# Kernel optimization log

Hardware: AMD Instinct MI355X
Metric: run time of the kernel (lower is better)

The kernel has to match this reference:

```python
import jax, jax.numpy as jnp
import numpy as np

B, N, F_IN, F_OUT, H = 4, 2048, 256, 256, 4
NEG_INF = -1e9
EDGE_PROB = 0.05
LEAKY_SLOPE = 0.2  # tf.nn.leaky_relu default alpha


def setup_inputs() -> dict:
    key = jax.random.key(0)
    k_x, k_m, k_w, k_a, k_b = jax.random.split(key, 5)
    inputs = jax.random.normal(k_x, (B, N, F_IN), dtype=jnp.float32)
    # bias: additive adjacency mask, 0 on edges / -1e9 off-edges (standard GAT)
    u = jax.random.uniform(k_m, (B, N, N), dtype=jnp.float32)
    bias = jnp.where(u < EDGE_PROB, 0.0, NEG_INF).astype(jnp.float32)
    # self-loops so every softmax row has at least one valid entry
    bias = bias.at[:, jnp.arange(N), jnp.arange(N)].set(0.0)
    # per-head learned params (uniform [0,1) init as in the original)
    W = jax.random.uniform(k_w, (H, F_IN, F_OUT), dtype=jnp.float32)
    a = jax.random.uniform(k_a, (H, F_OUT), dtype=jnp.float32)
    b = jax.random.uniform(k_b, (H, F_OUT), dtype=jnp.float32)
    return {"inputs": inputs, "bias": bias, "W": W, "a": a, "b": b}


def reference(inputs, bias, W, a, b):
    # transformed: [H, B, N, F_OUT]
    t = jnp.einsum('bnf,hfo->hbno', inputs, W) + b[:, None, None, :]
    # per-node score s = t @ a : [H, B, N]
    s = jnp.einsum('hbno,ho->hbn', t, a)
    # weights[i,j] = s[i] + s[j]  (weights + transpose)
    w = s[..., :, None] + s[..., None, :]  # [H, B, N, N]
    coefs = jax.nn.softmax(jax.nn.leaky_relu(w, negative_slope=LEAKY_SLOPE) + bias, axis=-1)
    heads = jnp.einsum('hbnm,hbmo->hbno', coefs, t)  # [H, B, N, F_OUT]
    return jnp.mean(heads, axis=0)  # (1/num_heads) * add_n(heads)
```

## Files before the change

### kernel.cpp

```cpp
#include <hip/hip_runtime.h>
#include <hip/hip_bf16.h>

#define H 4
#define BB 4
#define NN 2048
#define FIN 256
#define FOUT 256
#define M_TOT (BB*NN)
#define LEAKY 0.2f

typedef float f32x4 __attribute__((ext_vector_type(4)));
typedef short s16x8 __attribute__((ext_vector_type(8)));

static __device__ __forceinline__ short f2bf(float f) {
    return __builtin_bit_cast(short, __float2bfloat16(f));
}
static __device__ __forceinline__ float bf2f(short u) {
    unsigned x = ((unsigned)(unsigned short)u) << 16;
    return __builtin_bit_cast(float, x);
}

__global__ __launch_bounds__(256) void k_wt(const float* __restrict__ W, short* __restrict__ WT) {
    __shared__ float lds[64][65];
    int bid = blockIdx.x;
    int h = bid >> 4, kt = (bid >> 2) & 3, ot = bid & 3;
    int kb = kt * 64, ob = ot * 64;
    int tx = threadIdx.x & 63, ty = threadIdx.x >> 6;
#pragma unroll
    for (int r = 0; r < 16; ++r) {
        int k_l = ty + r * 4;
        lds[tx][k_l] = W[(size_t)(h * FIN + kb + k_l) * FOUT + ob + tx];
    }
    __syncthreads();
#pragma unroll
    for (int r = 0; r < 16; ++r) {
        int o_l = ty + r * 4;
        WT[(size_t)(h * FOUT + ob + o_l) * FIN + kb + tx] = f2bf(lds[o_l][tx]);
    }
}

__global__ __launch_bounds__(256) void k_q(const float* __restrict__ W, const float* __restrict__ a,
                                           float* __restrict__ q) {
    int wv = (blockIdx.x * 256 + threadIdx.x) >> 6;
    int lane = threadIdx.x & 63;
    int h = wv >> 8, f = wv & 255;
    float4 w4 = *(const float4*)(W + (size_t)(h * FIN + f) * FOUT + lane * 4);
    float4 a4 = *(const float4*)(a + h * FOUT + lane * 4);
    float d = w4.x * a4.x + w4.y * a4.y + w4.z * a4.z + w4.w * a4.w;
#pragma unroll
    for (int off = 32; off; off >>= 1) d += __shfl_xor(d, off);
    if (lane == 0) q[h * FIN + f] = d;
}

__global__ __launch_bounds__(256) void k_c(const float* __restrict__ bvec, const float* __restrict__ a,
                                           float* __restrict__ c) {
    int h = threadIdx.x >> 6, lane = threadIdx.x & 63;
    float4 b4 = *(const float4*)(bvec + h * FOUT + lane * 4);
    float4 a4 = *(const float4*)(a + h * FOUT + lane * 4);
    float d = b4.x * a4.x + b4.y * a4.y + b4.z * a4.z + b4.w * a4.w;
#pragma unroll
    for (int off = 32; off; off >>= 1) d += __shfl_xor(d, off);
    if (lane == 0) c[h] = d;
}

__global__ __launch_bounds__(256) void k_s(const float* __restrict__ X, const float* __restrict__ q,
                                           const float* __restrict__ c, float* __restrict__ s,
                                           short* __restrict__ Xbf) {
    int m = blockIdx.x * 4 + (threadIdx.x >> 6);
    int lane = threadIdx.x & 63;
    float4 xv = *(const float4*)(X + (size_t)m * FIN + lane * 4);
    short4 xb;
    xb.x = f2bf(xv.x); xb.y = f2bf(xv.y); xb.z = f2bf(xv.z); xb.w = f2bf(xv.w);
    *(short4*)(Xbf + (size_t)m * FIN + lane * 4) = xb;
#pragma unroll
    for (int h = 0; h < H; ++h) {
        float4 qv = *(const float4*)(q + h * FIN + lane * 4);
        float d = xv.x * qv.x + xv.y * qv.y + xv.z * qv.z + xv.w * qv.w;
#pragma unroll
        for (int off = 32; off; off >>= 1) d += __shfl_xor(d, off);
        if (lane == 0) s[h * M_TOT + m] = d + c[h];
    }
}

__global__ __launch_bounds__(256) void k_mask(const float* __restrict__ bias, unsigned* __restrict__ mask) {
    size_t t = (size_t)blockIdx.x * 256 + threadIdx.x;
    const float* p = bias + t * 32;
    unsigned bits = 0;
#pragma unroll
    for (int k = 0; k < 8; ++k) {
        float4 v = *(const float4*)(p + k * 4);
        bits |= (v.x > -1.f ? 1u : 0u) << (k * 4 + 0);
        bits |= (v.y > -1.f ? 1u : 0u) << (k * 4 + 1);
        bits |= (v.z > -1.f ? 1u : 0u) << (k * 4 + 2);
        bits |= (v.w > -1.f ? 1u : 0u) << (k * 4 + 3);
    }
    mask[t] = bits;
}

__global__ __launch_bounds__(256) void k_gemm_t(const short* __restrict__ WT, const short* __restrict__ Xbf,
                                                const float* __restrict__ bvec, short* __restrict__ tT) {
    int h = blockIdx.z;
    int ob = blockIdx.y * 64;
    int mb = blockIdx.x * 128;
    int lane = threadIdx.x & 63, w = threadIdx.x >> 6;
    int r16 = lane & 15, g = lane >> 4;
    int mw = mb + w * 32;
    f32x4 acc[4][2] = {};
    for (int k = 0; k < FIN; k += 32) {
        s16x8 afr[4], bfr[2];
#pragma unroll
        for (int fa = 0; fa < 4; ++fa)
            afr[fa] = *(const s16x8*)(WT + (size_t)(h * FOUT + ob + fa * 16 + r16) * FIN + k + g * 8);
#pragma unroll
        for (int fb = 0; fb < 2; ++fb)
            bfr[fb] = *(const s16x8*)(Xbf + (size_t)(mw + fb * 16 + r16) * FIN + k + g * 8);
#pragma unroll
        for (int fa = 0; fa < 4; ++fa)
#pragma unroll
            for (int fb = 0; fb < 2; ++fb)
                acc[fa][fb] = __builtin_amdgcn_mfma_f32_16x16x32_bf16(afr[fa], bfr[fb], acc[fa][fb], 0, 0, 0);
    }
#pragma unroll
    for (int fa = 0; fa < 4; ++fa) {
#pragma unroll
        for (int r = 0; r < 4; ++r) {
            int o = ob + fa * 16 + g * 4 + r;
            float bv = bvec[h * FOUT + o];
#pragma unroll
            for (int fb = 0; fb < 2; ++fb) {
                int m = mw + fb * 16 + r16;
                tT[(size_t)(h * FOUT + o) * M_TOT + m] = f2bf(acc[fa][fb][r] + bv);
            }
        }
    }
}

__global__ __launch_bounds__(512, 4) void k_attn(const short* __restrict__ tT, const float* __restrict__ s,
                                                 const unsigned* __restrict__ mask, short* __restrict__ OT) {
    __shared__ short lds_t[256 * 64];
    __shared__ float lds_ml[4][64][2];

    int flat = blockIdx.x + 32 * (blockIdx.y + 4 * blockIdx.z);
    int swz = (flat & 7) * 64 + (flat >> 3);
    int qt = swz & 31, b = (swz >> 5) & 3, h = swz >> 7;
    int ib = qt * 64;

    int tid = threadIdx.x;
    int lane = tid & 63, w = tid >> 6;
    int r16 = lane & 15, g = lane >> 4;
    int q16 = w >> 1, par = w & 1;
    int i_loc = ib + q16 * 16 + r16;
    size_t gm = (size_t)b * NN;

    float s_i = s[h * M_TOT + gm + i_loc];
    const float* srow = s + h * M_TOT + gm;
    const unsigned* mrowp = mask + ((size_t)(gm + i_loc)) * (NN / 32);

    int o_st = tid >> 1, hf = tid & 1;
    const short* src = tT + ((size_t)(h * FOUT) + o_st) * M_TOT + gm + hf * 32;
    int rd_base = r16 * 64 + ((((par << 2) + g) ^ (r16 & 7)) << 3);

    f32x4 acc[16] = {};
    float mrow = -1e9f, lrow = 0.f;

    s16x8 rv0 = *(const s16x8*)(src);
    s16x8 rv1 = *(const s16x8*)(src + 8);
    s16x8 rv2 = *(const s16x8*)(src + 16);
    s16x8 rv3 = *(const s16x8*)(src + 24);

    for (int it = 0; it < 32; ++it) {
        int wb = o_st * 64;
        int sw = (o_st & 7);
        *(s16x8*)(lds_t + wb + ((((hf << 2) + 0) ^ sw) << 3)) = rv0;
        *(s16x8*)(lds_t + wb + ((((hf << 2) + 1) ^ sw) << 3)) = rv1;
        *(s16x8*)(lds_t + wb + ((((hf << 2) + 2) ^ sw) << 3)) = rv2;
        *(s16x8*)(lds_t + wb + ((((hf << 2) + 3) ^ sw) << 3)) = rv3;
        __syncthreads();

        if (it + 1 < 32) {
            const short* nsrc = src + (it + 1) * 64;
            rv0 = *(const s16x8*)(nsrc);
            rv1 = *(const s16x8*)(nsrc + 8);
            rv2 = *(const s16x8*)(nsrc + 16);
            rv3 = *(const s16x8*)(nsrc + 24);
        }

        int jw = it * 64 + par * 32;
        unsigned mw = mrowp[jw >> 5];
        float4 sj0 = *(const float4*)(srow + jw + g * 8);
        float4 sj1 = *(const float4*)(srow + jw + g * 8 + 4);
        float sjv[8] = {sj0.x, sj0.y, sj0.z, sj0.w, sj1.x, sj1.y, sj1.z, sj1.w};
        float sc[8];
#pragma unroll
        for (int e = 0; e < 8; ++e) {
            float wv = s_i + sjv[e];
            float lv = wv > 0.f ? wv : LEAKY * wv;
            sc[e] = ((mw >> (g * 8 + e)) & 1u) ? lv : -1e9f;
        }
        float tmax = sc[0];
#pragma unroll
        for (int e = 1; e < 8; ++e) tmax = fmaxf(tmax, sc[e]);
        tmax = fmaxf(tmax, __shfl_xor(tmax, 16));
        tmax = fmaxf(tmax, __shfl_xor(tmax, 32));

        if (!__all(tmax <= mrow + 8.f)) {
            float mnew = fmaxf(mrow, tmax);
            float scale = __expf(mrow - mnew);
            lrow *= scale;
#pragma unroll
            for (int f = 0; f < 16; ++f) {
                acc[f][0] *= scale; acc[f][1] *= scale;
                acc[f][2] *= scale; acc[f][3] *= scale;
            }
            mrow = mnew;
        }

        float ps = 0.f;
        s16x8 pb;
#pragma unroll
        for (int e = 0; e < 8; ++e) {
            float p = ((mw >> (g * 8 + e)) & 1u) ? __expf(sc[e] - mrow) : 0.f;
            ps += p;
            pb[e] = f2bf(p);
        }
        ps += __shfl_xor(ps, 16);
        ps += __shfl_xor(ps, 32);
        lrow += ps;

#pragma unroll
        for (int f = 0; f < 16; ++f) {
            s16x8 af = *(const s16x8*)(lds_t + f * 1024 + rd_base);
            acc[f] = __builtin_amdgcn_mfma_f32_16x16x32_bf16(af, pb, acc[f], 0, 0, 0);
        }
        __syncthreads();
    }

    if (par) {
        lds_ml[q16][lane][0] = mrow;
        lds_ml[q16][lane][1] = lrow;
    }
    __syncthreads();
    float f0 = 0.f, f1 = 0.f;
    if (!par) {
        float m1 = lds_ml[q16][lane][0];
        float l1 = lds_ml[q16][lane][1];
        float ms = fmaxf(mrow, m1);
        float s0 = __expf(mrow - ms);
        float s1 = __expf(m1 - ms);
        float ln = lrow * s0 + l1 * s1;
        float inv = 1.f / ln;
        f0 = s0 * inv; f1 = s1 * inv;
    }
    f32x4* accst = (f32x4*)lds_t;
#pragma unroll
    for (int r = 0; r < 2; ++r) {
        if (par) {
#pragma unroll
            for (int f = 0; f < 8; ++f) accst[(q16 * 8 + f) * 64 + lane] = acc[r * 8 + f];
        }
        __syncthreads();
        if (!par) {
#pragma unroll
            for (int f = 0; f < 8; ++f) {
                f32x4 v1 = accst[(q16 * 8 + f) * 64 + lane];
                f32x4 v = acc[r * 8 + f] * f0 + v1 * f1;
                int fg = r * 8 + f;
#pragma unroll
                for (int rr = 0; rr < 4; ++rr) {
                    int o = fg * 16 + g * 4 + rr;
                    OT[(size_t)(h * FOUT + o) * M_TOT + gm + i_loc] = f2bf(v[rr]);
                }
            }
        }
        __syncthreads();
    }
}

__global__ __launch_bounds__(256) void k_reduce(const short* __restrict__ OT, float* __restrict__ out) {
    __shared__ float lds[32][72];
    int mb = blockIdx.x * 64, obt = blockIdx.y * 32;
    int tid = threadIdx.x;
    {
        int o_l = tid >> 3;
        int m_l = (tid & 7) * 8;
        float acc[8] = {};
#pragma unroll
        for (int h = 0; h < H; ++h) {
            s16x8 v = *(const s16x8*)(OT + (size_t)(h * FOUT + obt + o_l) * M_TOT + mb + m_l);
#pragma unroll
            for (int e = 0; e < 8; ++e) acc[e] += bf2f(v[e]);
        }
#pragma unroll
        for (int e = 0; e < 8; ++e) lds[o_l][m_l + e] = acc[e] * 0.25f;
    }
    __syncthreads();
    {
        int m_l = tid >> 2;
        int o_l = (tid & 3) * 8;
        float4 v0, v1;
        v0.x = lds[o_l + 0][m_l]; v0.y = lds[o_l + 1][m_l];
        v0.z = lds[o_l + 2][m_l]; v0.w = lds[o_l + 3][m_l];
        v1.x = lds[o_l + 4][m_l]; v1.y = lds[o_l + 5][m_l];
        v1.z = lds[o_l + 6][m_l]; v1.w = lds[o_l + 7][m_l];
        float* dst = out + (size_t)(mb + m_l) * FOUT + obt + o_l;
        *(float4*)dst = v0;
        *(float4*)(dst + 4) = v1;
    }
}

extern "C" void kernel_launch(void* const* d_in, const int* in_sizes, int n_in,
                              void* d_out, int out_size, void* d_ws, size_t ws_size,
                              hipStream_t stream) {
    const float* X    = (const float*)d_in[0];
    const float* bias = (const float*)d_in[1];
    const float* W    = (const float*)d_in[2];
    const float* a    = (const float*)d_in[3];
    const float* bvec = (const float*)d_in[4];
    float* out = (float*)d_out;

    char* ws = (char*)d_ws;
    short*    Xbf  = (short*)ws;
    short*    WT   = (short*)(ws + (4u << 20));
    float*    q    = (float*)(ws + (4u << 20) + (768u << 10));
    float*    c    = q + H * FIN;
    float*    s    = (float*)(ws + (5u << 20));
    short*    tT   = (short*)(ws + (6u << 20));
    short*    OT   = (short*)(ws + (22u << 20));
    unsigned* mask = (unsigned*)(ws + (38u << 20));

    k_wt<<<64, 256, 0, stream>>>(W, WT);
    k_q<<<256, 256, 0, stream>>>(W, a, q);
    k_c<<<1, 256, 0, stream>>>(bvec, a, c);
    k_s<<<2048, 256, 0, stream>>>(X, q, c, s, Xbf);
    k_mask<<<2048, 256, 0, stream>>>(bias, mask);
    k_gemm_t<<<dim3(64, 4, 4), 256, 0, stream>>>(WT, Xbf, bvec, tT);
    k_attn<<<dim3(32, 4, 4), 512, 0, stream>>>(tT, s, mask, OT);
    k_reduce<<<dim3(128, 8), 256, 0, stream>>>(OT, out);
}
```

Baseline: 142.8 us.

## Double-buffer attention K tiles via direct global-to-LDS loads with pre-swizzled layout

The GEMM now writes the transformed features into a pre-tiled, XOR-swizzled slab layout so the attention kernel can copy each 64-column tile straight into LDS with global_load_lds. Those copies are double-buffered so the next tile loads while MFMAs run on the current one. The block shrinks from 512 to 256 threads, and each wave now handles two 16-row query groups that share each LDS fragment load. This raises register pressure (two accumulator sets), uses more LDS for the double buffer, and lowers occupancy.

After: 139.3 us. -2.5%, faster.

```diff
diff --git a/kernel.cpp b/kernel.cpp
--- a/kernel.cpp
+++ b/kernel.cpp
@@ -1,5 +1,6 @@
 #include <hip/hip_runtime.h>
 #include <hip/hip_bf16.h>
+#include <stdint.h>
 
 #define H 4
 #define BB 4
@@ -11,6 +12,7 @@
 
 typedef float f32x4 __attribute__((ext_vector_type(4)));
 typedef short s16x8 __attribute__((ext_vector_type(8)));
+typedef unsigned int u32;
 
 static __device__ __forceinline__ short f2bf(float f) {
     return __builtin_bit_cast(short, __float2bfloat16(f));
@@ -18,6 +20,16 @@
 static __device__ __forceinline__ float bf2f(short u) {
     unsigned x = ((unsigned)(unsigned short)u) << 16;
     return __builtin_bit_cast(float, x);
+}
+static __device__ __forceinline__ void glds16(const void* g, void* l) {
+    __builtin_amdgcn_global_load_lds(
+        (const __attribute__((address_space(1))) u32*)(g),
+        (__attribute__((address_space(3))) u32*)(l), 16, 0, 0);
+}
+
+static __device__ __forceinline__ size_t tts_addr(int h, int b, int o, int j) {
+    return ((size_t)((h * 4 + b) * 32 + (j >> 6))) * 16384
+         + o * 64 + ((((j >> 3) & 7) ^ (o & 7)) << 3) + (j & 7);
 }
 
 __global__ __launch_bounds__(256) void k_wt(const float* __restrict__ W, short* __restrict__ WT) {
@@ -98,7 +110,7 @@
 }
 
 __global__ __launch_bounds__(256) void k_gemm_t(const short* __restrict__ WT, const short* __restrict__ Xbf,
-                                                const float* __restrict__ bvec, short* __restrict__ tT) {
+                                                const float* __restrict__ bvec, short* __restrict__ tTs) {
     int h = blockIdx.z;
     int ob = blockIdx.y * 64;
     int mb = blockIdx.x * 128;
@@ -129,16 +141,17 @@
 #pragma unroll
             for (int fb = 0; fb < 2; ++fb) {
                 int m = mw + fb * 16 + r16;
-                tT[(size_t)(h * FOUT + o) * M_TOT + m] = f2bf(acc[fa][fb][r] + bv);
+                int bb = m >> 11, j = m & 2047;
+                tTs[tts_addr(h, bb, o, j)] = f2bf(acc[fa][fb][r] + bv);
             }
         }
     }
 }
 
-__global__ __launch_bounds__(512, 4) void k_attn(const short* __restrict__ tT, const float* __restrict__ s,
+__global__ __launch_bounds__(256, 2) void k_attn(const short* __restrict__ tTs, const float* __restrict__ s,
                                                  const unsigned* __restrict__ mask, short* __restrict__ OT) {
-    __shared__ short lds_t[256 * 64];
-    __shared__ float lds_ml[4][64][2];
+    __shared__ short buf[2][16384];
+    __shared__ float lds_ml[2][64][4];
 
     int flat = blockIdx.x + 32 * (blockIdx.y + 4 * blockIdx.z);
     int swz = (flat & 7) * 64 + (flat >> 3);
@@ -148,131 +161,139 @@
     int tid = threadIdx.x;
     int lane = tid & 63, w = tid >> 6;
     int r16 = lane & 15, g = lane >> 4;
-    int q16 = w >> 1, par = w & 1;
-    int i_loc = ib + q16 * 16 + r16;
+    int qg = w >> 1, par = w & 1;
+    int i0 = ib + qg * 32 + r16, i1 = i0 + 16;
     size_t gm = (size_t)b * NN;
 
-    float s_i = s[h * M_TOT + gm + i_loc];
+    const char* slab = (const char*)(tTs + (size_t)(h * 4 + b) * 32 * 16384);
+    float si0 = s[h * M_TOT + gm + i0];
+    float si1 = s[h * M_TOT + gm + i1];
     const float* srow = s + h * M_TOT + gm;
-    const unsigned* mrowp = mask + ((size_t)(gm + i_loc)) * (NN / 32);
-
-    int o_st = tid >> 1, hf = tid & 1;
-    const short* src = tT + ((size_t)(h * FOUT) + o_st) * M_TOT + gm + hf * 32;
+    const unsigned* mk0 = mask + (gm + i0) * (NN / 32);
+    const unsigned* mk1 = mask + (gm + i1) * (NN / 32);
+
     int rd_base = r16 * 64 + ((((par << 2) + g) ^ (r16 & 7)) << 3);
 
-    f32x4 acc[16] = {};
-    float mrow = -1e9f, lrow = 0.f;
-
-    s16x8 rv0 = *(const s16x8*)(src);
-    s16x8 rv1 = *(const s16x8*)(src + 8);
-    s16x8 rv2 = *(const s16x8*)(src + 16);
-    s16x8 rv3 = *(const s16x8*)(src + 24);
-
-    for (int it = 0; it < 32; ++it) {
-        int wb = o_st * 64;
-        int sw = (o_st & 7);
-        *(s16x8*)(lds_t + wb + ((((hf << 2) + 0) ^ sw) << 3)) = rv0;
-        *(s16x8*)(lds_t + wb + ((((hf << 2) + 1) ^ sw) << 3)) = rv1;
-        *(s16x8*)(lds_t + wb + ((((hf << 2) + 2) ^ sw) << 3)) = rv2;
-        *(s16x8*)(lds_t + wb + ((((hf << 2) + 3) ^ sw) << 3)) = rv3;
-        __syncthreads();
-
-        if (it + 1 < 32) {
-            const short* nsrc = src + (it + 1) * 64;
-            rv0 = *(const s16x8*)(nsrc);
-            rv1 = *(const s16x8*)(nsrc + 8);
-            rv2 = *(const s16x8*)(nsrc + 16);
-            rv3 = *(const s16x8*)(nsrc + 24);
-        }
-
-        int jw = it * 64 + par * 32;
-        unsigned mw = mrowp[jw >> 5];
+    f32x4 acc[16][2] = {};
+    float m0 = -1e9f, l0 = 0.f, m1 = -1e9f, l1 = 0.f;
+
+    {
+        const char* gsrc = slab + w * 8192 + lane * 16;
+#pragma unroll
+        for (int k = 0; k < 8; ++k)
+            glds16(gsrc + k * 1024, &buf[0][w * 4096 + k * 512]);
+    }
+    asm volatile("s_waitcnt vmcnt(0)" ::: "memory");
+    __builtin_amdgcn_s_barrier();
+    __builtin_amdgcn_sched_barrier(0);
+
+    for (int t = 0; t < 32; ++t) {
+        int cur = t & 1;
+        int jw = t * 64 + par * 32;
         float4 sj0 = *(const float4*)(srow + jw + g * 8);
         float4 sj1 = *(const float4*)(srow + jw + g * 8 + 4);
-        float sjv[8] = {sj0.x, sj0.y, sj0.z, sj0.w, sj1.x, sj1.y, sj1.z, sj1.w};
-        float sc[8];
+        unsigned w0 = mk0[t * 2 + par] >> (g * 8);
+        unsigned w1 = mk1[t * 2 + par] >> (g * 8);
+        float sj[8] = {sj0.x, sj0.y, sj0.z, sj0.w, sj1.x, sj1.y, sj1.z, sj1.w};
+        float sc0[8], sc1[8];
 #pragma unroll
         for (int e = 0; e < 8; ++e) {
-            float wv = s_i + sjv[e];
-            float lv = wv > 0.f ? wv : LEAKY * wv;
-            sc[e] = ((mw >> (g * 8 + e)) & 1u) ? lv : -1e9f;
-        }
-        float tmax = sc[0];
-#pragma unroll
-        for (int e = 1; e < 8; ++e) tmax = fmaxf(tmax, sc[e]);
-        tmax = fmaxf(tmax, __shfl_xor(tmax, 16));
-        tmax = fmaxf(tmax, __shfl_xor(tmax, 32));
-
-        if (!__all(tmax <= mrow + 8.f)) {
-            float mnew = fmaxf(mrow, tmax);
-            float scale = __expf(mrow - mnew);
-            lrow *= scale;
-#pragma unroll
-            for (int f = 0; f < 16; ++f) {
-                acc[f][0] *= scale; acc[f][1] *= scale;
-                acc[f][2] *= scale; acc[f][3] *= scale;
+            float y0 = si0 + sj[e];
+            float y1 = si1 + sj[e];
+            float ly0 = fmaxf(y0, 0.2f * y0);
+            float ly1 = fmaxf(y1, 0.2f * y1);
+            sc0[e] = ((w0 >> e) & 1u) ? ly0 : -1e9f;
+            sc1[e] = ((w1 >> e) & 1u) ? ly1 : -1e9f;
+        }
+        float t0 = fmaxf(fmaxf(fmaxf(sc0[0], sc0[1]), fmaxf(sc0[2], sc0[3])),
+                         fmaxf(fmaxf(sc0[4], sc0[5]), fmaxf(sc0[6], sc0[7])));
+        float t1 = fmaxf(fmaxf(fmaxf(sc1[0], sc1[1]), fmaxf(sc1[2], sc1[3])),
+                         fmaxf(fmaxf(sc1[4], sc1[5]), fmaxf(sc1[6], sc1[7])));
+        t0 = fmaxf(t0, __shfl_xor(t0, 16)); t0 = fmaxf(t0, __shfl_xor(t0, 32));
+        t1 = fmaxf(t1, __shfl_xor(t1, 16)); t1 = fmaxf(t1, __shfl_xor(t1, 32));
+
+        if (!__all((t0 <= m0 + 8.f) && (t1 <= m1 + 8.f))) {
+            float mn0 = fmaxf(m0, t0), mn1 = fmaxf(m1, t1);
+            float s0 = __expf(m0 - mn0), s1 = __expf(m1 - mn1);
+            l0 *= s0; l1 *= s1;
+#pragma unroll
+            for (int f = 0; f < 16; ++f) { acc[f][0] *= s0; acc[f][1] *= s1; }
+            m0 = mn0; m1 = mn1;
+        }
+
+        float ps0 = 0.f, ps1 = 0.f;
+        s16x8 pb0, pb1;
+#pragma unroll
+        for (int e = 0; e < 8; ++e) {
+            float p0 = __expf(sc0[e] - m0);
+            float p1 = __expf(sc1[e] - m1);
+            ps0 += p0; ps1 += p1;
+            pb0[e] = f2bf(p0); pb1[e] = f2bf(p1);
+        }
+        ps0 += __shfl_xor(ps0, 16); ps0 += __shfl_xor(ps0, 32);
+        ps1 += __shfl_xor(ps1, 16); ps1 += __shfl_xor(ps1, 32);
+        l0 += ps0; l1 += ps1;
+
+        __builtin_amdgcn_sched_barrier(0);
+        if (t + 1 < 32) {
+            const char* gsrc = slab + (size_t)(t + 1) * 32768 + w * 8192 + lane * 16;
+#pragma unroll
+            for (int k = 0; k < 8; ++k)
+                glds16(gsrc + k * 1024, &buf[cur ^ 1][w * 4096 + k * 512]);
+        }
+        asm volatile("s_waitcnt vmcnt(8)" ::: "memory");
+        __builtin_amdgcn_s_barrier();
+        __builtin_amdgcn_sched_barrier(0);
+
+        const short* bp = &buf[cur][0];
+        __builtin_amdgcn_s_setprio(1);
+#pragma unroll
+        for (int f = 0; f < 16; ++f) {
+            s16x8 af = *(const s16x8*)(bp + f * 1024 + rd_base);
+            acc[f][0] = __builtin_amdgcn_mfma_f32_16x16x32_bf16(af, pb0, acc[f][0], 0, 0, 0);
+            acc[f][1] = __builtin_amdgcn_mfma_f32_16x16x32_bf16(af, pb1, acc[f][1], 0, 0, 0);
+        }
+        __builtin_amdgcn_s_setprio(0);
+        __builtin_amdgcn_sched_barrier(0);
+        __builtin_amdgcn_s_barrier();
+    }
+
+    if (par) {
+        lds_ml[qg][lane][0] = m0; lds_ml[qg][lane][1] = l0;
+        lds_ml[qg][lane][2] = m1; lds_ml[qg][lane][3] = l1;
+    }
+    f32x4* ex = (f32x4*)buf;
+    if (par) {
+#pragma unroll
+        for (int f = 0; f < 16; ++f) {
+            ex[((qg * 16 + f) * 2 + 0) * 64 + lane] = acc[f][0];
+            ex[((qg * 16 + f) * 2 + 1) * 64 + lane] = acc[f][1];
+        }
+    }
+    __syncthreads();
+    if (!par) {
+        float mo0 = lds_ml[qg][lane][0], lo0 = lds_ml[qg][lane][1];
+        float mo1 = lds_ml[qg][lane][2], lo1 = lds_ml[qg][lane][3];
+        float ms0 = fmaxf(m0, mo0);
+        float a0 = __expf(m0 - ms0), b0 = __expf(mo0 - ms0);
+        float inv0 = 1.f / (l0 * a0 + lo0 * b0);
+        float w00 = a0 * inv0, w01 = b0 * inv0;
+        float ms1 = fmaxf(m1, mo1);
+        float a1 = __expf(m1 - ms1), b1 = __expf(mo1 - ms1);
+        float inv1 = 1.f / (l1 * a1 + lo1 * b1);
+        float w10 = a1 * inv1, w11 = b1 * inv1;
+        size_t ob0 = (size_t)h * FOUT * M_TOT + gm;
+#pragma unroll
+        for (int f = 0; f < 16; ++f) {
+            f32x4 v0 = acc[f][0] * w00 + ex[((qg * 16 + f) * 2 + 0) * 64 + lane] * w01;
+            f32x4 v1 = acc[f][1] * w10 + ex[((qg * 16 + f) * 2 + 1) * 64 + lane] * w11;
+#pragma unroll
+            for (int rr = 0; rr < 4; ++rr) {
+                int o = f * 16 + g * 4 + rr;
+                OT[ob0 + (size_t)o * M_TOT + i0] = f2bf(v0[rr]);
+                OT[ob0 + (size_t)o * M_TOT + i1] = f2bf(v1[rr]);
             }
-            mrow = mnew;
-        }
-
-        float ps = 0.f;
-        s16x8 pb;
-#pragma unroll
-        for (int e = 0; e < 8; ++e) {
-            float p = ((mw >> (g * 8 + e)) & 1u) ? __expf(sc[e] - mrow) : 0.f;
-            ps += p;
-            pb[e] = f2bf(p);
-        }
-        ps += __shfl_xor(ps, 16);
-        ps += __shfl_xor(ps, 32);
-        lrow += ps;
-
-#pragma unroll
-        for (int f = 0; f < 16; ++f) {
-            s16x8 af = *(const s16x8*)(lds_t + f * 1024 + rd_base);
-            acc[f] = __builtin_amdgcn_mfma_f32_16x16x32_bf16(af, pb, acc[f], 0, 0, 0);
-        }
-        __syncthreads();
-    }
-
-    if (par) {
-        lds_ml[q16][lane][0] = mrow;
-        lds_ml[q16][lane][1] = lrow;
-    }
-    __syncthreads();
-    float f0 = 0.f, f1 = 0.f;
-    if (!par) {
-        float m1 = lds_ml[q16][lane][0];
-        float l1 = lds_ml[q16][lane][1];
-        float ms = fmaxf(mrow, m1);
-        float s0 = __expf(mrow - ms);
-        float s1 = __expf(m1 - ms);
-        float ln = lrow * s0 + l1 * s1;
-        float inv = 1.f / ln;
-        f0 = s0 * inv; f1 = s1 * inv;
-    }
-    f32x4* accst = (f32x4*)lds_t;
-#pragma unroll
-    for (int r = 0; r < 2; ++r) {
-        if (par) {
-#pragma unroll
-            for (int f = 0; f < 8; ++f) accst[(q16 * 8 + f) * 64 + lane] = acc[r * 8 + f];
-        }
-        __syncthreads();
-        if (!par) {
-#pragma unroll
-            for (int f = 0; f < 8; ++f) {
-                f32x4 v1 = accst[(q16 * 8 + f) * 64 + lane];
-                f32x4 v = acc[r * 8 + f] * f0 + v1 * f1;
-                int fg = r * 8 + f;
-#pragma unroll
-                for (int rr = 0; rr < 4; ++rr) {
-                    int o = fg * 16 + g * 4 + rr;
-                    OT[(size_t)(h * FOUT + o) * M_TOT + gm + i_loc] = f2bf(v[rr]);
-                }
-            }
-        }
-        __syncthreads();
+        }
     }
 }
 
@@ -324,7 +345,7 @@
     float*    q    = (float*)(ws + (4u << 20) + (768u << 10));
     float*    c    = q + H * FIN;
     float*    s    = (float*)(ws + (5u << 20));
-    short*    tT   = (short*)(ws + (6u << 20));
+    short*    tTs  = (short*)(ws + (6u << 20));
     short*    OT   = (short*)(ws + (22u << 20));
     unsigned* mask = (unsigned*)(ws + (38u << 20));
 
@@ -333,7 +354,7 @@
     k_c<<<1, 256, 0, stream>>>(bvec, a, c);
     k_s<<<2048, 256, 0, stream>>>(X, q, c, s, Xbf);
     k_mask<<<2048, 256, 0, stream>>>(bias, mask);
-    k_gemm_t<<<dim3(64, 4, 4), 256, 0, stream>>>(WT, Xbf, bvec, tT);
-    k_attn<<<dim3(32, 4, 4), 512, 0, stream>>>(tT, s, mask, OT);
+    k_gemm_t<<<dim3(64, 4, 4), 256, 0, stream>>>(WT, Xbf, bvec, tTs);
+    k_attn<<<dim3(32, 4, 4), 256, 0, stream>>>(tTs, s, mask, OT);
     k_reduce<<<dim3(128, 8), 256, 0, stream>>>(OT, out);
 }
```
